# Kernel tuning notes

Hardware: AMD Instinct MI355X
Metric: run time of the kernel (lower is better)

The kernel has to match this reference:

```python
import jax, jax.numpy as jnp
import numpy as np

B, NX, NY = 4, 16384, 16384
CX = CY = 256
CK = CV = 256
H = 8


def setup_inputs() -> dict:
    key = jax.random.key(0)
    ks = jax.random.split(key, 12)
    s = 0.02
    return {
        "x": jax.random.normal(ks[0], (B, NX, CX), jnp.float32),
        "y": jax.random.normal(ks[1], (B, NY, CY), jnp.float32),
        "x_pos_embed": jax.random.normal(ks[2], (B, NX, CX), jnp.float32),
        "y_pos_embed": jax.random.normal(ks[3], (B, NY, CY), jnp.float32),
        "Wq": jax.random.normal(ks[4], (CK, CX), jnp.float32) * s,
        "bq": jnp.zeros((CK,), jnp.float32),
        "Wk": jax.random.normal(ks[5], (CK, CY), jnp.float32) * s,
        "bk": jnp.zeros((CK,), jnp.float32),
        "Wv": jax.random.normal(ks[6], (CV, CY), jnp.float32) * s,
        "bv": jnp.zeros((CV,), jnp.float32),
        "Wr": jax.random.normal(ks[7], (CX, CV), jnp.float32) * s,
        "br": jnp.zeros((CX,), jnp.float32),
    }


def reference(x, y, x_pos_embed, y_pos_embed, Wq, bq, Wk, bk, Wv, bv, Wr, br):
    # Linear projections (nn.Linear: x @ W.T + b)
    q = (x + x_pos_embed) @ Wq.T + bq            # [B, Nx, Ck]
    k = (y + y_pos_embed) @ Wk.T + bk            # [B, Ny, Ck]
    v = y @ Wv.T + bv                            # [B, Ny, Cv]

    dk, dv = CK // H, CV // H
    # Split heads: [B, N, H, d] -> [B, H, N, d]
    q = q.reshape(B, NX, H, dk).transpose(0, 2, 1, 3)
    k = k.reshape(B, NY, H, dk).transpose(0, 2, 1, 3)
    v = v.reshape(B, NY, H, dv).transpose(0, 2, 1, 3)

    # key softmax over tokens (Ny); query softmax over per-head channels (dk)
    k = jax.nn.softmax(k, axis=2)                # [B, H, Ny, dk]
    q = jax.nn.softmax(q, axis=3)                # [B, H, Nx, dk]

    # context = softmax(K)^T V : [B, H, dk, dv]
    context = jnp.einsum('bhnk,bhnv->bhkv', k, v)
    # attended = Q context : [B, H, Nx, dv]
    attended = jnp.einsum('bhnk,bhkv->bhnv', q, context)

    # merge heads -> [B, Nx, Cv], reproject -> [B, Nx, Cx]
    agg = attended.transpose(0, 2, 1, 3).reshape(B, NX, CV)
    return agg @ Wr.T + br
```

## Files before the change

### kernel.cpp

```cpp
#include <hip/hip_runtime.h>


typedef float f32x4 __attribute__((ext_vector_type(4)));
typedef short s16x4 __attribute__((ext_vector_type(4)));
typedef short s16x8 __attribute__((ext_vector_type(8)));

#define MFMA16(A, B, C) __builtin_amdgcn_mfma_f32_16x16x32_bf16((A), (B), (C), 0, 0, 0)

__device__ __forceinline__ short f2bf(float f) {
    unsigned u = __builtin_bit_cast(unsigned, f);
    u = (u + 0x7FFFu + ((u >> 16) & 1u)) >> 16;
    return (short)u;
}
__device__ __forceinline__ float bf2f(short b) {
    unsigned u = ((unsigned)(unsigned short)b) << 16;
    return __builtin_bit_cast(float, u);
}

__global__ __launch_bounds__(256) void wcvt_kernel(
    const float* __restrict__ wq, const float* __restrict__ wk,
    const float* __restrict__ wv, const float* __restrict__ wr,
    short* __restrict__ wbf)
{
    int id = blockIdx.x * 256 + threadIdx.x;
    int m = id >> 13;
    int slot = id & 8191;
    int tile = slot >> 9;
    int ks   = (slot >> 6) & 7;
    int lane = slot & 63;
    int lrow = lane & 15, lgrp = lane >> 4;
    const float* src = (m == 0) ? wq : (m == 1) ? wk : (m == 2) ? wv : wr;
    const float* p = src + (size_t)(tile * 16 + lrow) * 256 + ks * 32 + lgrp * 8;
    f32x4 a = *(const f32x4*)p;
    f32x4 b = *(const f32x4*)(p + 4);
    s16x8 o;
    o[0]=f2bf(a[0]); o[1]=f2bf(a[1]); o[2]=f2bf(a[2]); o[3]=f2bf(a[3]);
    o[4]=f2bf(b[0]); o[5]=f2bf(b[1]); o[6]=f2bf(b[2]); o[7]=f2bf(b[3]);
    *(s16x8*)(wbf + (size_t)id * 8) = o;
}

__global__ __launch_bounds__(256) void kv_kernel(
    const float* __restrict__ y, const float* __restrict__ ypos,
    const short* __restrict__ wkp, const short* __restrict__ wvp,
    const float* __restrict__ bk, const float* __restrict__ bv,
    short* __restrict__ e_buf, short* __restrict__ v_buf)
{
    __shared__ short smem[32 * 512];
    short* ak = smem;
    short* av = smem + 32 * 256;
    const int row0 = blockIdx.x * 32;
    const int t = threadIdx.x;
    const int w = t >> 6, lane = t & 63;

    {
        f32x4 ly[8], lp[8];
        #pragma unroll
        for (int it = 0; it < 8; ++it) {
            int r = it * 4 + w;
            ly[it] = *(const f32x4*)(y    + (size_t)(row0 + r) * 256 + lane * 4);
            lp[it] = *(const f32x4*)(ypos + (size_t)(row0 + r) * 256 + lane * 4);
        }
        #pragma unroll
        for (int it = 0; it < 8; ++it) {
            int r = it * 4 + w;
            f32x4 a = ly[it];
            f32x4 k = a + lp[it];
            s16x4 ov, ok;
            ov[0]=f2bf(a[0]); ov[1]=f2bf(a[1]); ov[2]=f2bf(a[2]); ov[3]=f2bf(a[3]);
            ok[0]=f2bf(k[0]); ok[1]=f2bf(k[1]); ok[2]=f2bf(k[2]); ok[3]=f2bf(k[3]);
            int swz = ((lane >> 1) ^ (r & 7)) * 8 + (lane & 1) * 4;
            *(s16x4*)(av + r * 256 + swz) = ov;
            *(s16x4*)(ak + r * 256 + swz) = ok;
        }
    }
    __syncthreads();

    const int lrow = lane & 15, lgrp = lane >> 4;
    const bool is_k = (w < 2);
    const int colbase = (w & 1) * 128;
    const int tile0 = colbase >> 4;
    const short* WP = is_k ? wkp : wvp;
    const float* bp = is_k ? bk : bv;
    const short* A = is_k ? ak : av;

    float bias[8];
    #pragma unroll
    for (int nf = 0; nf < 8; ++nf) bias[nf] = bp[colbase + nf * 16 + lrow];

    s16x8 af[2][8];
    #pragma unroll
    for (int mf = 0; mf < 2; ++mf) {
        int rr = mf * 16 + lrow;
        #pragma unroll
        for (int ks = 0; ks < 8; ++ks) {
            int cs = ((ks * 4 + lgrp) ^ (rr & 7));
            af[mf][ks] = *(const s16x8*)(A + rr * 256 + cs * 8);
        }
    }
    __syncthreads();

    const short* wt = WP + lane * 8;
    s16x8 bf[2][8];
    #pragma unroll
    for (int k = 0; k < 8; ++k)
        bf[0][k] = *(const s16x8*)(wt + ((size_t)tile0 * 8 + k) * 512);

    #pragma unroll
    for (int nf = 0; nf < 8; ++nf) {
        const int cur = nf & 1, nxt = cur ^ 1;
        if (nf < 7) {
            #pragma unroll
            for (int k = 0; k < 8; ++k)
                bf[nxt][k] = *(const s16x8*)(wt + ((size_t)(tile0 + nf + 1) * 8 + k) * 512);
        }
        f32x4 a0 = (f32x4){0.f, 0.f, 0.f, 0.f};
        f32x4 a1 = (f32x4){0.f, 0.f, 0.f, 0.f};
        #pragma unroll
        for (int k = 0; k < 8; ++k) {
            a0 = MFMA16(af[0][k], bf[cur][k], a0);
            a1 = MFMA16(af[1][k], bf[cur][k], a1);
        }
        const int colp = (is_k ? 0 : 256) + colbase + nf * 16 + lrow;
        #pragma unroll
        for (int rr = 0; rr < 4; ++rr) {
            float v0 = a0[rr] + bias[nf];
            float v1 = a1[rr] + bias[nf];
            if (is_k) { v0 = __expf(v0); v1 = __expf(v1); }
            int lr0 = lgrp * 4 + rr;
            int lr1 = lr0 + 16;
            smem[lr0 * 512 + (((colp >> 3) ^ (lr0 & 7)) * 8) + (colp & 7)] = f2bf(v0);
            smem[lr1 * 512 + (((colp >> 3) ^ (lr1 & 7)) * 8) + (colp & 7)] = f2bf(v1);
        }
    }
    __syncthreads();

    {
        #pragma unroll
        for (int i = 0; i < 8; ++i) {
            int r = i * 4 + w;
            int grow = row0 + r;
            s16x8 val = *(const s16x8*)(smem + r * 512 + (lane ^ (r & 7)) * 8);
            if (lane < 32)
                *(s16x8*)(e_buf + (size_t)grow * 256 + lane * 8) = val;
            else
                *(s16x8*)(v_buf + (size_t)grow * 256 + (lane - 32) * 8) = val;
        }
    }
}

__global__ __launch_bounds__(256) void ctx_kernel(
    const short* __restrict__ e_buf, const short* __restrict__ v_buf,
    float* __restrict__ partials)
{
    __shared__ float se[128 * 32];
    __shared__ float sv[128 * 32];
    __shared__ float red[4 * 1056];
    const int cb = blockIdx.x, bh = blockIdx.y;
    const int b = bh >> 3, h = bh & 7;
    const int tok0 = b * 16384 + cb * 1024;
    const int t = threadIdx.x, w = t >> 6, lane = t & 63;
    const int ckb = (lane >> 3) * 4, cvb = (lane & 7) * 4;

    f32x4 acc[4];
    #pragma unroll
    for (int i = 0; i < 4; ++i) acc[i] = (f32x4){0.f, 0.f, 0.f, 0.f};
    f32x4 dn = (f32x4){0.f, 0.f, 0.f, 0.f};

    for (int it = 0; it < 8; ++it) {
        __syncthreads();
        #pragma unroll
        for (int s = 0; s < 2; ++s) {
            int id = t + s * 256;
            int rr = id >> 2, pp = id & 3;
            size_t g = (size_t)(tok0 + it * 128 + rr) * 256 + h * 32 + pp * 8;
            s16x8 ee = *(const s16x8*)(e_buf + g);
            s16x8 vv = *(const s16x8*)(v_buf + g);
            f32x4 e0 = {bf2f(ee[0]), bf2f(ee[1]), bf2f(ee[2]), bf2f(ee[3])};
            f32x4 e1 = {bf2f(ee[4]), bf2f(ee[5]), bf2f(ee[6]), bf2f(ee[7])};
            f32x4 v0 = {bf2f(vv[0]), bf2f(vv[1]), bf2f(vv[2]), bf2f(vv[3])};
            f32x4 v1 = {bf2f(vv[4]), bf2f(vv[5]), bf2f(vv[6]), bf2f(vv[7])};
            *(f32x4*)(se + rr * 32 + pp * 8)     = e0;
            *(f32x4*)(se + rr * 32 + pp * 8 + 4) = e1;
            *(f32x4*)(sv + rr * 32 + pp * 8)     = v0;
            *(f32x4*)(sv + rr * 32 + pp * 8 + 4) = v1;
        }
        __syncthreads();
        const int r0 = w * 32;
        #pragma unroll 8
        for (int rr = 0; rr < 32; ++rr) {
            f32x4 e4 = *(const f32x4*)(se + (r0 + rr) * 32 + ckb);
            f32x4 v4 = *(const f32x4*)(sv + (r0 + rr) * 32 + cvb);
            acc[0] += e4[0] * v4;
            acc[1] += e4[1] * v4;
            acc[2] += e4[2] * v4;
            acc[3] += e4[3] * v4;
            dn += e4;
        }
    }
    __syncthreads();
    #pragma unroll
    for (int i = 0; i < 4; ++i)
        *(f32x4*)(red + w * 1056 + (ckb + i) * 32 + cvb) = acc[i];
    if ((lane & 7) == 0)
        *(f32x4*)(red + w * 1056 + 1024 + ckb) = dn;
    __syncthreads();
    float* outp = partials + (size_t)(bh * 16 + cb) * 1056;
    for (int e = t; e < 1056; e += 256)
        outp[e] = red[e] + red[1056 + e] + red[2112 + e] + red[3168 + e];
}

__global__ __launch_bounds__(256) void ctx_reduce_kernel(
    const float* __restrict__ partials, short* __restrict__ ctxT)
{
    __shared__ float s[1056];
    const int bh = blockIdx.x, t = threadIdx.x;
    for (int e = t; e < 1056; e += 256) {
        float a = 0.f;
        for (int c = 0; c < 16; ++c) a += partials[(size_t)(bh * 16 + c) * 1056 + e];
        s[e] = a;
    }
    __syncthreads();
    for (int e = t; e < 1024; e += 256) {
        int ck = e >> 5, cv = e & 31;
        float val = s[e] / s[1024 + ck];
        ctxT[(size_t)bh * 1024 + cv * 32 + ck] = f2bf(val);
    }
}

__global__ __launch_bounds__(256) void qout_kernel(
    const float* __restrict__ x, const float* __restrict__ xpos,
    const short* __restrict__ wqp, const float* __restrict__ bq,
    const short* __restrict__ ctxT,
    const short* __restrict__ wrp, const float* __restrict__ br,
    float* __restrict__ out)
{
    __shared__ short alds[32 * 256];
    __shared__ short qlds[4][32 * 64];
    const int row0 = blockIdx.x * 32;
    const int b = row0 >> 14;
    const int t = threadIdx.x;
    const int w = t >> 6, lane = t & 63;

    {
        f32x4 lx[8], lp[8];
        #pragma unroll
        for (int it = 0; it < 8; ++it) {
            int r = it * 4 + w;
            lx[it] = *(const f32x4*)(x    + (size_t)(row0 + r) * 256 + lane * 4);
            lp[it] = *(const f32x4*)(xpos + (size_t)(row0 + r) * 256 + lane * 4);
        }
        #pragma unroll
        for (int it = 0; it < 8; ++it) {
            int r = it * 4 + w;
            f32x4 a = lx[it] + lp[it];
            s16x4 o;
            o[0]=f2bf(a[0]); o[1]=f2bf(a[1]); o[2]=f2bf(a[2]); o[3]=f2bf(a[3]);
            int swz = ((lane >> 1) ^ (r & 7)) * 8 + (lane & 1) * 4;
            *(s16x4*)(alds + r * 256 + swz) = o;
        }
    }
    __syncthreads();

    const int lrow = lane & 15, lgrp = lane >> 4;
    const int wc = w * 64;
    const int tile0 = wc >> 4;

    float biasq[4];
    #pragma unroll
    for (int nf = 0; nf < 4; ++nf) biasq[nf] = bq[wc + nf * 16 + lrow];

    f32x4 acc[2][4];
    #pragma unroll
    for (int mf = 0; mf < 2; ++mf)
        #pragma unroll
        for (int nf = 0; nf < 4; ++nf) acc[mf][nf] = (f32x4){0.f, 0.f, 0.f, 0.f};

    {
        const short* wq8 = wqp + lane * 8;
        s16x8 bfq[2][4];
        #pragma unroll
        for (int nf = 0; nf < 4; ++nf)
            bfq[0][nf] = *(const s16x8*)(wq8 + ((size_t)(tile0 + nf) * 8 + 0) * 512);
        #pragma unroll
        for (int ks = 0; ks < 8; ++ks) {
            const int cur = ks & 1, nxt = cur ^ 1;
            if (ks < 7) {
                #pragma unroll
                for (int nf = 0; nf < 4; ++nf)
                    bfq[nxt][nf] = *(const s16x8*)(wq8 + ((size_t)(tile0 + nf) * 8 + ks + 1) * 512);
            }
            s16x8 af[2];
            #pragma unroll
            for (int mf = 0; mf < 2; ++mf) {
                int rr = mf * 16 + lrow;
                int cs = (ks * 4 + lgrp) ^ (rr & 7);
                af[mf] = *(const s16x8*)(alds + rr * 256 + cs * 8);
            }
            #pragma unroll
            for (int nf = 0; nf < 4; ++nf) {
                acc[0][nf] = MFMA16(af[0], bfq[cur][nf], acc[0][nf]);
                acc[1][nf] = MFMA16(af[1], bfq[cur][nf], acc[1][nf]);
            }
        }
    }

    short* ql = (short*)qlds[w];
    #pragma unroll
    for (int mf = 0; mf < 2; ++mf) {
        f32x4 e[4];
        #pragma unroll
        for (int nf = 0; nf < 4; ++nf)
            #pragma unroll
            for (int rr = 0; rr < 4; ++rr)
                e[nf][rr] = __expf(acc[mf][nf][rr] + biasq[nf]);
        #pragma unroll
        for (int hl = 0; hl < 2; ++hl) {
            #pragma unroll
            for (int rr = 0; rr < 4; ++rr) {
                float s = e[hl * 2][rr] + e[hl * 2 + 1][rr];
                s += __shfl_xor(s, 1);
                s += __shfl_xor(s, 2);
                s += __shfl_xor(s, 4);
                s += __shfl_xor(s, 8);
                float rinv = 1.0f / s;
                int row = mf * 16 + lgrp * 4 + rr;
                #pragma unroll
                for (int n2 = 0; n2 < 2; ++n2) {
                    int colc = hl * 32 + n2 * 16 + lrow;
                    int cs = (colc >> 3) ^ (row & 7);
                    ql[row * 64 + cs * 8 + (colc & 7)] = f2bf(e[hl * 2 + n2][rr] * rinv);
                }
            }
        }
    }
    __syncthreads();

    f32x4 att[2][2][2];
    #pragma unroll
    for (int hl = 0; hl < 2; ++hl)
        #pragma unroll
        for (int mf = 0; mf < 2; ++mf)
            #pragma unroll
            for (int n2 = 0; n2 < 2; ++n2) att[hl][mf][n2] = (f32x4){0.f,0.f,0.f,0.f};

    #pragma unroll
    for (int hl = 0; hl < 2; ++hl) {
        const short* cbase = ctxT + (size_t)(b * 8 + w * 2 + hl) * 1024;
        s16x8 bctx[2];
        #pragma unroll
        for (int n2 = 0; n2 < 2; ++n2)
            bctx[n2] = *(const s16x8*)(cbase + (n2 * 16 + lrow) * 32 + lgrp * 8);
        #pragma unroll
        for (int mf = 0; mf < 2; ++mf) {
            int row = mf * 16 + lrow;
            int cs = (hl * 4 + lgrp) ^ (row & 7);
            s16x8 aq = *(const s16x8*)(ql + row * 64 + cs * 8);
            #pragma unroll
            for (int n2 = 0; n2 < 2; ++n2)
                att[hl][mf][n2] = MFMA16(aq, bctx[n2], att[hl][mf][n2]);
        }
    }

    #pragma unroll
    for (int hl = 0; hl < 2; ++hl)
      #pragma unroll
      for (int mf = 0; mf < 2; ++mf)
        #pragma unroll
        for (int n2 = 0; n2 < 2; ++n2)
          #pragma unroll
          for (int rr = 0; rr < 4; ++rr) {
              int row = mf * 16 + lgrp * 4 + rr;
              int col = wc + hl * 32 + n2 * 16 + lrow;
              int cs = (col >> 3) ^ (row & 7);
              alds[row * 256 + cs * 8 + (col & 7)] = f2bf(att[hl][mf][n2][rr]);
          }
    __syncthreads();

    float biasr[4];
    #pragma unroll
    for (int nf = 0; nf < 4; ++nf) biasr[nf] = br[wc + nf * 16 + lrow];

    f32x4 acc2[2][4];
    #pragma unroll
    for (int mf = 0; mf < 2; ++mf)
        #pragma unroll
        for (int nf = 0; nf < 4; ++nf) acc2[mf][nf] = (f32x4){0.f, 0.f, 0.f, 0.f};

    {
        const short* wr8 = wrp + lane * 8;
        s16x8 bfr[2][4];
        #pragma unroll
        for (int nf = 0; nf < 4; ++nf)
            bfr[0][nf] = *(const s16x8*)(wr8 + ((size_t)(tile0 + nf) * 8 + 0) * 512);
        #pragma unroll
        for (int ks = 0; ks < 8; ++ks) {
            const int cur = ks & 1, nxt = cur ^ 1;
            if (ks < 7) {
                #pragma unroll
                for (int nf = 0; nf < 4; ++nf)
                    bfr[nxt][nf] = *(const s16x8*)(wr8 + ((size_t)(tile0 + nf) * 8 + ks + 1) * 512);
            }
            s16x8 af[2];
            #pragma unroll
            for (int mf = 0; mf < 2; ++mf) {
                int rr = mf * 16 + lrow;
                int cs = (ks * 4 + lgrp) ^ (rr & 7);
                af[mf] = *(const s16x8*)(alds + rr * 256 + cs * 8);
            }
            #pragma unroll
            for (int nf = 0; nf < 4; ++nf) {
                acc2[0][nf] = MFMA16(af[0], bfr[cur][nf], acc2[0][nf]);
                acc2[1][nf] = MFMA16(af[1], bfr[cur][nf], acc2[1][nf]);
            }
        }
    }

    #pragma unroll
    for (int mf = 0; mf < 2; ++mf)
      #pragma unroll
      for (int nf = 0; nf < 4; ++nf)
        #pragma unroll
        for (int rr = 0; rr < 4; ++rr) {
            int grow = row0 + mf * 16 + lgrp * 4 + rr;
            out[(size_t)grow * 256 + wc + nf * 16 + lrow] = acc2[mf][nf][rr] + biasr[nf];
        }
}

extern "C" void kernel_launch(void* const* d_in, const int* in_sizes, int n_in,
                              void* d_out, int out_size, void* d_ws, size_t ws_size,
                              hipStream_t stream)
{
    const float* x    = (const float*)d_in[0];
    const float* y    = (const float*)d_in[1];
    const float* xpos = (const float*)d_in[2];
    const float* ypos = (const float*)d_in[3];
    const float* Wq   = (const float*)d_in[4];
    const float* bq   = (const float*)d_in[5];
    const float* Wk   = (const float*)d_in[6];
    const float* bk   = (const float*)d_in[7];
    const float* Wv   = (const float*)d_in[8];
    const float* bv   = (const float*)d_in[9];
    const float* Wr   = (const float*)d_in[10];
    const float* br   = (const float*)d_in[11];

    char*  ws    = (char*)d_ws;
    short* wbf   = (short*)(ws);
    short* ctxT  = (short*)(ws + 524288);
    float* parts = (float*)(ws + (1 << 20));
    short* e_buf = (short*)(ws + ((size_t)4 << 20));
    short* v_buf = e_buf + (size_t)65536 * 256;
    float* outp  = (float*)d_out;

    hipLaunchKernelGGL(wcvt_kernel, dim3(128), dim3(256), 0, stream,
                       Wq, Wk, Wv, Wr, wbf);
    hipLaunchKernelGGL(kv_kernel, dim3(2048), dim3(256), 0, stream,
                       y, ypos, wbf + 65536, wbf + 131072, bk, bv, e_buf, v_buf);
    hipLaunchKernelGGL(ctx_kernel, dim3(16, 32), dim3(256), 0, stream,
                       e_buf, v_buf, parts);
    hipLaunchKernelGGL(ctx_reduce_kernel, dim3(32), dim3(256), 0, stream,
                       parts, ctxT);
    hipLaunchKernelGGL(qout_kernel, dim3(2048), dim3(256), 0, stream,
                       x, xpos, wbf, bq, ctxT, wbf + 196608, br, outp);
}
```

Measured before the change: 168.6 us.

## Use nontemporal loads/stores, stage output through LDS, simplify weight prefetch

Streaming inputs and intermediate e/v buffers now use nontemporal loads and stores so they do not pollute the cache. The final output is staged through a swizzled LDS tile so each row is written with coalesced 16-byte stores instead of scattered scalar stores. The kv kernel drops the double-buffered register weight prefetch in favour of smaller per-group loads and gets a launch-bounds occupancy hint. Together these lower register pressure and improve write coalescing, but they remove latency hiding for weight loads and add two barriers to the output kernel.

```diff
diff --git a/kernel.cpp b/kernel.cpp
--- a/kernel.cpp
+++ b/kernel.cpp
@@ -15,6 +15,18 @@
 __device__ __forceinline__ float bf2f(short b) {
     unsigned u = ((unsigned)(unsigned short)b) << 16;
     return __builtin_bit_cast(float, u);
+}
+__device__ __forceinline__ f32x4 ntld4f(const float* p) {
+    return __builtin_nontemporal_load((const f32x4*)p);
+}
+__device__ __forceinline__ s16x8 ntld8s(const short* p) {
+    return __builtin_nontemporal_load((const s16x8*)p);
+}
+__device__ __forceinline__ void ntst8s(short* p, s16x8 v) {
+    __builtin_nontemporal_store(v, (s16x8*)p);
+}
+__device__ __forceinline__ void ntst4f(float* p, f32x4 v) {
+    __builtin_nontemporal_store(v, (f32x4*)p);
 }
 
 __global__ __launch_bounds__(256) void wcvt_kernel(
@@ -39,7 +51,7 @@
     *(s16x8*)(wbf + (size_t)id * 8) = o;
 }
 
-__global__ __launch_bounds__(256) void kv_kernel(
+__global__ __launch_bounds__(256, 4) void kv_kernel(
     const float* __restrict__ y, const float* __restrict__ ypos,
     const short* __restrict__ wkp, const short* __restrict__ wvp,
     const float* __restrict__ bk, const float* __restrict__ bv,
@@ -53,18 +65,12 @@
     const int w = t >> 6, lane = t & 63;
 
     {
-        f32x4 ly[8], lp[8];
         #pragma unroll
         for (int it = 0; it < 8; ++it) {
             int r = it * 4 + w;
-            ly[it] = *(const f32x4*)(y    + (size_t)(row0 + r) * 256 + lane * 4);
-            lp[it] = *(const f32x4*)(ypos + (size_t)(row0 + r) * 256 + lane * 4);
-        }
-        #pragma unroll
-        for (int it = 0; it < 8; ++it) {
-            int r = it * 4 + w;
-            f32x4 a = ly[it];
-            f32x4 k = a + lp[it];
+            f32x4 a = ntld4f(y    + (size_t)(row0 + r) * 256 + lane * 4);
+            f32x4 p = ntld4f(ypos + (size_t)(row0 + r) * 256 + lane * 4);
+            f32x4 k = a + p;
             s16x4 ov, ok;
             ov[0]=f2bf(a[0]); ov[1]=f2bf(a[1]); ov[2]=f2bf(a[2]); ov[3]=f2bf(a[3]);
             ok[0]=f2bf(k[0]); ok[1]=f2bf(k[1]); ok[2]=f2bf(k[2]); ok[3]=f2bf(k[3]);
@@ -99,26 +105,23 @@
     }
     __syncthreads();
 
-    const short* wt = WP + lane * 8;
-    s16x8 bf[2][8];
-    #pragma unroll
-    for (int k = 0; k < 8; ++k)
-        bf[0][k] = *(const s16x8*)(wt + ((size_t)tile0 * 8 + k) * 512);
-
     #pragma unroll
     for (int nf = 0; nf < 8; ++nf) {
-        const int cur = nf & 1, nxt = cur ^ 1;
-        if (nf < 7) {
-            #pragma unroll
-            for (int k = 0; k < 8; ++k)
-                bf[nxt][k] = *(const s16x8*)(wt + ((size_t)(tile0 + nf + 1) * 8 + k) * 512);
-        }
+        const int tile = tile0 + nf;
+        const short* wt = WP + ((size_t)tile * 8) * 512 + lane * 8;
         f32x4 a0 = (f32x4){0.f, 0.f, 0.f, 0.f};
         f32x4 a1 = (f32x4){0.f, 0.f, 0.f, 0.f};
         #pragma unroll
-        for (int k = 0; k < 8; ++k) {
-            a0 = MFMA16(af[0][k], bf[cur][k], a0);
-            a1 = MFMA16(af[1][k], bf[cur][k], a1);
+        for (int kg = 0; kg < 2; ++kg) {
+            s16x8 bf[4];
+            #pragma unroll
+            for (int kk = 0; kk < 4; ++kk)
+                bf[kk] = *(const s16x8*)(wt + (kg * 4 + kk) * 512);
+            #pragma unroll
+            for (int kk = 0; kk < 4; ++kk) {
+                a0 = MFMA16(af[0][kg * 4 + kk], bf[kk], a0);
+                a1 = MFMA16(af[1][kg * 4 + kk], bf[kk], a1);
+            }
         }
         const int colp = (is_k ? 0 : 256) + colbase + nf * 16 + lrow;
         #pragma unroll
@@ -139,11 +142,11 @@
         for (int i = 0; i < 8; ++i) {
             int r = i * 4 + w;
             int grow = row0 + r;
-            s16x8 val = *(const s16x8*)(smem + r * 512 + (lane ^ (r & 7)) * 8);
+            s16x8 val = *(const s16x8*)(smem + r * 512 + ((lane ^ (r & 7)) << 3));
             if (lane < 32)
-                *(s16x8*)(e_buf + (size_t)grow * 256 + lane * 8) = val;
+                ntst8s(e_buf + (size_t)grow * 256 + lane * 8, val);
             else
-                *(s16x8*)(v_buf + (size_t)grow * 256 + (lane - 32) * 8) = val;
+                ntst8s(v_buf + (size_t)grow * 256 + (lane - 32) * 8, val);
         }
     }
 }
@@ -173,8 +176,8 @@
             int id = t + s * 256;
             int rr = id >> 2, pp = id & 3;
             size_t g = (size_t)(tok0 + it * 128 + rr) * 256 + h * 32 + pp * 8;
-            s16x8 ee = *(const s16x8*)(e_buf + g);
-            s16x8 vv = *(const s16x8*)(v_buf + g);
+            s16x8 ee = ntld8s(e_buf + g);
+            s16x8 vv = ntld8s(v_buf + g);
             f32x4 e0 = {bf2f(ee[0]), bf2f(ee[1]), bf2f(ee[2]), bf2f(ee[3])};
             f32x4 e1 = {bf2f(ee[4]), bf2f(ee[5]), bf2f(ee[6]), bf2f(ee[7])};
             f32x4 v0 = {bf2f(vv[0]), bf2f(vv[1]), bf2f(vv[2]), bf2f(vv[3])};
@@ -234,8 +237,8 @@
     const short* __restrict__ wrp, const float* __restrict__ br,
     float* __restrict__ out)
 {
-    __shared__ short alds[32 * 256];
-    __shared__ short qlds[4][32 * 64];
+    __shared__ short smem[32 * 512];
+    short* alds = smem;
     const int row0 = blockIdx.x * 32;
     const int b = row0 >> 14;
     const int t = threadIdx.x;
@@ -246,8 +249,8 @@
         #pragma unroll
         for (int it = 0; it < 8; ++it) {
             int r = it * 4 + w;
-            lx[it] = *(const f32x4*)(x    + (size_t)(row0 + r) * 256 + lane * 4);
-            lp[it] = *(const f32x4*)(xpos + (size_t)(row0 + r) * 256 + lane * 4);
+            lx[it] = ntld4f(x    + (size_t)(row0 + r) * 256 + lane * 4);
+            lp[it] = ntld4f(xpos + (size_t)(row0 + r) * 256 + lane * 4);
         }
         #pragma unroll
         for (int it = 0; it < 8; ++it) {
@@ -304,7 +307,7 @@
         }
     }
 
-    short* ql = (short*)qlds[w];
+    short* ql = smem + 8192 + w * 2048;
     #pragma unroll
     for (int mf = 0; mf < 2; ++mf) {
         f32x4 e[4];
@@ -414,16 +417,28 @@
             }
         }
     }
-
+    __syncthreads();
+
+    float* cf = (float*)smem;
     #pragma unroll
     for (int mf = 0; mf < 2; ++mf)
       #pragma unroll
       for (int nf = 0; nf < 4; ++nf)
         #pragma unroll
         for (int rr = 0; rr < 4; ++rr) {
-            int grow = row0 + mf * 16 + lgrp * 4 + rr;
-            out[(size_t)grow * 256 + wc + nf * 16 + lrow] = acc2[mf][nf][rr] + biasr[nf];
-        }
+            int row = mf * 16 + lgrp * 4 + rr;
+            int col = wc + nf * 16 + lrow;
+            int chunk = col >> 2, pos = col & 3;
+            cf[row * 256 + ((chunk ^ (row & 7)) << 2) + pos] = acc2[mf][nf][rr] + biasr[nf];
+        }
+    __syncthreads();
+
+    #pragma unroll
+    for (int i = 0; i < 8; ++i) {
+        int r = i * 4 + w;
+        f32x4 val = *(const f32x4*)(cf + r * 256 + (((lane ^ (r & 7)) & 63) << 2));
+        ntst4f(out + (size_t)(row0 + r) * 256 + lane * 4, val);
+    }
 }
 
 extern "C" void kernel_launch(void* const* d_in, const int* in_sizes, int n_in,
```

Result: faster. 158.7 us (median of 3 runs) (-5.9%).
